# Optimization experiments

Measured on AMD Instinct MI355X. Metric: run time of the kernel, lower is better.

## Reference

```python
import jax, jax.numpy as jnp
import numpy as np

DIM = 768
NUM_HEADS = 12
HEAD_DIM = DIM // NUM_HEADS
B, N = 16, 784


def setup_inputs() -> dict:
    key = jax.random.key(0)
    k1, k2, k3, k4, k5 = jax.random.split(key, 5)
    x = jax.random.normal(k1, (B, N, DIM), dtype=jnp.float32)
    # Dense params (flax Dense: kernel [in, out], bias [out])
    Wqkv = jax.random.normal(k2, (DIM, 3 * DIM), dtype=jnp.float32) * (DIM ** -0.5)
    bqkv = jnp.zeros((3 * DIM,), dtype=jnp.float32)
    Wo = jax.random.normal(k3, (DIM, DIM), dtype=jnp.float32) * (DIM ** -0.5)
    bo = jnp.zeros((DIM,), dtype=jnp.float32)
    return {"x": x, "Wqkv": Wqkv, "bqkv": bqkv, "Wo": Wo, "bo": bo}


def reference(x, Wqkv, bqkv, Wo, bo):
    b, n, dim = x.shape
    # fused QKV projection
    qkv = jnp.einsum('bnd,df->bnf', x, Wqkv) + bqkv          # [b, n, 3*dim]
    qkv = qkv.reshape(b, n, 3, NUM_HEADS, HEAD_DIM)           # '(k h d)' split
    q, k, v = qkv[:, :, 0], qkv[:, :, 1], qkv[:, :, 2]        # [b, n, h, d]
    scale = HEAD_DIM ** -0.5
    # chunked/flash path computes exact softmax attention; same math, expressed densely
    scores = jnp.einsum('bihd,bjhd->bhij', q, k) * scale      # [b, h, n, n]
    attn = jax.nn.softmax(scores, axis=-1)
    out = jnp.einsum('bhij,bjhd->bihd', attn, v)              # [b, n, h, d]
    out = out.reshape(b, n, dim)                              # 'b n (h d)'
    return jnp.einsum('bnd,df->bnf', out, Wo) + bo
```

## Files before the change

kernel.cpp:

```cpp
#include <hip/hip_runtime.h>

#define DIM 768
#define NHEADS 12
#define HDIM 64
#define BB 16
#define NN 784
#define M_TOTAL (BB * NN)

typedef __attribute__((ext_vector_type(8))) _Float16 f16x8;
typedef __attribute__((ext_vector_type(4))) float f32x4;
typedef __attribute__((ext_vector_type(16))) float f32x16;

typedef __attribute__((address_space(3))) unsigned int lds_uint;
typedef __attribute__((address_space(1))) const unsigned int g_uint;
__device__ inline void gload_lds16(const void* g, void* l) {
    __builtin_amdgcn_global_load_lds((g_uint*)(uintptr_t)g,
                                     (lds_uint*)(uintptr_t)l, 16, 0, 0);
}

__global__ __launch_bounds__(256) void cvt_f16_kernel(
    const float* __restrict__ in, _Float16* __restrict__ out, int n)
{
    int i = (blockIdx.x * 256 + threadIdx.x) * 8;
    if (i >= n) return;
    float4 a = *(const float4*)&in[i];
    float4 b = *(const float4*)&in[i + 4];
    union { _Float16 h[8]; uint4 v; } o;
    o.h[0] = (_Float16)a.x; o.h[1] = (_Float16)a.y;
    o.h[2] = (_Float16)a.z; o.h[3] = (_Float16)a.w;
    o.h[4] = (_Float16)b.x; o.h[5] = (_Float16)b.y;
    o.h[6] = (_Float16)b.z; o.h[7] = (_Float16)b.w;
    *(uint4*)&out[i] = o.v;
}

__global__ __launch_bounds__(256) void transpose_f16_kernel(
    const float* __restrict__ W, _Float16* __restrict__ T, int K, int N)
{
    __shared__ float t[32][33];
    const int n0 = blockIdx.x * 32, k0 = blockIdx.y * 32;
    const int r = threadIdx.x >> 3, c4 = (threadIdx.x & 7) * 4;
    float4 v = *(const float4*)&W[(size_t)(k0 + r) * N + n0 + c4];
    t[r][c4 + 0] = v.x; t[r][c4 + 1] = v.y;
    t[r][c4 + 2] = v.z; t[r][c4 + 3] = v.w;
    __syncthreads();
    union { _Float16 h[4]; ushort4 v4; } o;
#pragma unroll
    for (int i = 0; i < 4; ++i) o.h[i] = (_Float16)t[c4 + i][r];
    *(ushort4*)&T[(size_t)(n0 + r) * K + k0 + c4] = o.v4;
}

template <int OUT_F16>
__global__ __launch_bounds__(256) void gemm_f16_kernel(
    const _Float16* __restrict__ A, const _Float16* __restrict__ B,
    const float* __restrict__ bias, void* __restrict__ Cout,
    int M, int N, int K)
{
    __shared__ _Float16 sA[128 * 64];
    __shared__ _Float16 sB[128 * 64];

    const int tid  = threadIdx.x;
    const int wave = tid >> 6;
    const int lane = tid & 63;
    const int gm = blockIdx.y * 128;
    const int gn = blockIdx.x * 128;
    const int wm = (wave & 1) * 64;
    const int wn = (wave >> 1) * 64;
    const int l31 = lane & 31;
    const int hi  = lane >> 5;

    const int srow = lane >> 3;
    const int scol = (((lane & 7) ^ (srow & 7)) * 8);

    f32x16 acc[2][2] = {};

    for (int k0 = 0; k0 < K; k0 += 64) {
        __syncthreads();
#pragma unroll
        for (int i = 0; i < 4; ++i) {
            const int rbase = wave * 32 + i * 8;
            gload_lds16(A + (size_t)(gm + rbase + srow) * K + k0 + scol,
                        &sA[rbase * 64]);
            gload_lds16(B + (size_t)(gn + rbase + srow) * K + k0 + scol,
                        &sB[rbase * 64]);
        }
        __syncthreads();

#pragma unroll
        for (int kk = 0; kk < 4; ++kk) {
            const int c = kk * 2 + hi;
            const int sw = (c ^ (l31 & 7)) * 8;
            f16x8 a[2], bf[2];
#pragma unroll
            for (int mt = 0; mt < 2; ++mt)
                a[mt] = *(const f16x8*)&sA[(wm + mt * 32 + l31) * 64 + sw];
#pragma unroll
            for (int nt = 0; nt < 2; ++nt)
                bf[nt] = *(const f16x8*)&sB[(wn + nt * 32 + l31) * 64 + sw];
#pragma unroll
            for (int mt = 0; mt < 2; ++mt)
#pragma unroll
                for (int nt = 0; nt < 2; ++nt)
                    acc[mt][nt] = __builtin_amdgcn_mfma_f32_32x32x16_f16(
                        a[mt], bf[nt], acc[mt][nt], 0, 0, 0);
        }
    }

#pragma unroll
    for (int nt = 0; nt < 2; ++nt) {
        const int col = gn + wn + nt * 32 + l31;
        const float bv = bias[col];
#pragma unroll
        for (int mt = 0; mt < 2; ++mt) {
            f32x16 v = acc[mt][nt];
#pragma unroll
            for (int reg = 0; reg < 16; ++reg) {
                const int row = gm + wm + mt * 32 + (reg & 3) + 8 * (reg >> 2) + 4 * hi;
                const float o = v[reg] + bv;
                if (OUT_F16)
                    ((_Float16*)Cout)[(size_t)row * N + col] = (_Float16)o;
                else
                    ((float*)Cout)[(size_t)row * N + col] = o;
            }
        }
    }
}

#define LOG2E_8 0.18033688f

#define ATTN_TILE(J0, TAIL)                                                    \
  {                                                                            \
    const int j0_ = (J0);                                                      \
    int jrowK = j0_ + sj;                                                      \
    if (TAIL && jrowK > NN - 1) jrowK = NN - 1;                                \
    const size_t kbase = (size_t)(b * NN + jrowK) * (3 * DIM) + DIM + h * HDIM;\
    uint4 k0v = *(const uint4*)&qkv[kbase + sg * 8];                           \
    uint4 k1v = *(const uint4*)&qkv[kbase + sg * 8 + 32];                      \
    int vr0 = j0_ + 2 * jj, vr1 = j0_ + 2 * jj + 1;                            \
    if (TAIL) { if (vr0 > NN - 1) vr0 = NN - 1; if (vr1 > NN - 1) vr1 = NN - 1; } \
    const size_t vb0 = (size_t)(b * NN + vr0) * (3 * DIM) + 2 * DIM + h * HDIM + dsub; \
    const size_t vb1 = (size_t)(b * NN + vr1) * (3 * DIM) + 2 * DIM + h * HDIM + dsub; \
    union { uint4 v; _Float16 h[8]; } va, vc;                                  \
    va.v = *(const uint4*)&qkv[vb0];                                           \
    vc.v = *(const uint4*)&qkv[vb1];                                           \
    __syncthreads();                                                           \
    *(uint4*)&Ks[sj][sg * 8]      = k0v;                                       \
    *(uint4*)&Ks[sj][sg * 8 + 32] = k1v;                                       \
    _Pragma("unroll")                                                          \
    for (int i = 0; i < 8; ++i) {                                              \
        union { _Float16 h[2]; unsigned int u; } t;                            \
        t.h[0] = va.h[i]; t.h[1] = vc.h[i];                                    \
        *(unsigned int*)&Vt[dsub + i][2 * jj] = t.u;                           \
    }                                                                          \
    __syncthreads();                                                           \
    f32x4 s[4] = {};                                                           \
    _Pragma("unroll")                                                          \
    for (int nt = 0; nt < 4; ++nt) {                                           \
        f16x8 kf0 = *(const f16x8*)&Ks[nt * 16 + l16][quad * 8];               \
        f16x8 kf1 = *(const f16x8*)&Ks[nt * 16 + l16][32 + quad * 8];          \
        s[nt] = __builtin_amdgcn_mfma_f32_16x16x32_f16(qfrag[0], kf0, s[nt], 0, 0, 0); \
        s[nt] = __builtin_amdgcn_mfma_f32_16x16x32_f16(qfrag[1], kf1, s[nt], 0, 0, 0); \
    }                                                                          \
    _Pragma("unroll")                                                          \
    for (int nt = 0; nt < 4; ++nt)                                             \
        _Pragma("unroll")                                                      \
        for (int r = 0; r < 4; ++r) {                                          \
            float pv = exp2f(s[nt][r]);                                        \
            if (TAIL && (j0_ + nt * 16) >= NN) pv = 0.f;                       \
            lpart[r] += pv;                                                    \
            Ph[wave * 16 + quad * 4 + r][nt * 16 + l16] = (_Float16)pv;        \
        }                                                                      \
    _Pragma("unroll")                                                          \
    for (int ks = 0; ks < 2; ++ks) {                                           \
        f16x8 ph = *(const f16x8*)&Ph[wave * 16 + l16][ks * 32 + quad * 8];    \
        _Pragma("unroll")                                                      \
        for (int dt = 0; dt < 4; ++dt) {                                       \
            f16x8 vf = *(const f16x8*)&Vt[dt * 16 + l16][ks * 32 + quad * 8];  \
            O[dt] = __builtin_amdgcn_mfma_f32_16x16x32_f16(ph, vf, O[dt], 0, 0, 0); \
        }                                                                      \
    }                                                                          \
  }

__global__ __launch_bounds__(256) void attn_f16_kernel(
    const _Float16* __restrict__ qkv, _Float16* __restrict__ oat)
{
    const int b = blockIdx.z;
    const int h = blockIdx.y;
    const int q0 = blockIdx.x * 64;
    const int tid = threadIdx.x;
    const int wave = tid >> 6;
    const int lane = tid & 63;
    const int quad = lane >> 4;
    const int l16  = lane & 15;

    __shared__ _Float16 Ks[64][72];
    __shared__ _Float16 Vt[64][72];
    __shared__ _Float16 Ph[64][72];

    f16x8 qfrag[2];
    {
        int qrow = q0 + wave * 16 + l16; if (qrow > NN - 1) qrow = NN - 1;
        size_t base = (size_t)(b * NN + qrow) * (3 * DIM) + h * HDIM;
        f16x8 q0v = *(const f16x8*)&qkv[base + quad * 8];
        f16x8 q1v = *(const f16x8*)&qkv[base + 32 + quad * 8];
        qfrag[0] = q0v * (_Float16)LOG2E_8;
        qfrag[1] = q1v * (_Float16)LOG2E_8;
    }

    const int sj = lane;
    const int sg = wave;
    const int jj   = lane & 31;
    const int dsub = sg * 16 + (lane >> 5) * 8;

    f32x4 O[4] = {};
    float lpart[4] = {};

    for (int jt = 0; jt < 12; ++jt) {
        ATTN_TILE(jt * 64, 0)
    }
    ATTN_TILE(768, 1)

    float lrow[4];
#pragma unroll
    for (int r = 0; r < 4; ++r) {
        float t = lpart[r];
        t += __shfl_xor(t, 1);
        t += __shfl_xor(t, 2);
        t += __shfl_xor(t, 4);
        t += __shfl_xor(t, 8);
        lrow[r] = t;
    }

#pragma unroll
    for (int r = 0; r < 4; ++r) {
        const int q = q0 + wave * 16 + quad * 4 + r;
        if (q < NN) {
            const float inv = 1.0f / lrow[r];
#pragma unroll
            for (int dt = 0; dt < 4; ++dt) {
                const size_t base = (size_t)(b * NN + q) * DIM + h * HDIM + dt * 16 + l16;
                oat[base] = (_Float16)(O[dt][r] * inv);
            }
        }
    }
}

extern "C" void kernel_launch(void* const* d_in, const int* in_sizes, int n_in,
                              void* d_out, int out_size, void* d_ws, size_t ws_size,
                              hipStream_t stream) {
    const float* x    = (const float*)d_in[0];
    const float* Wqkv = (const float*)d_in[1];
    const float* bqkv = (const float*)d_in[2];
    const float* Wo   = (const float*)d_in[3];
    const float* bo   = (const float*)d_in[4];
    float* out = (float*)d_out;

    _Float16* qkv = (_Float16*)d_ws;
    _Float16* xh  = qkv + (size_t)M_TOTAL * 3 * DIM;
    _Float16* wqT = xh + (size_t)M_TOTAL * DIM;
    _Float16* woT = wqT + (size_t)3 * DIM * DIM;
    _Float16* oat = xh;

    {
        int n = M_TOTAL * DIM;
        cvt_f16_kernel<<<n / 8 / 256, 256, 0, stream>>>(x, xh, n);
    }
    transpose_f16_kernel<<<dim3((3 * DIM) / 32, DIM / 32), 256, 0, stream>>>(
        Wqkv, wqT, DIM, 3 * DIM);
    transpose_f16_kernel<<<dim3(DIM / 32, DIM / 32), 256, 0, stream>>>(
        Wo, woT, DIM, DIM);
    gemm_f16_kernel<1><<<dim3((3 * DIM) / 128, M_TOTAL / 128), 256, 0, stream>>>(
        xh, wqT, bqkv, qkv, M_TOTAL, 3 * DIM, DIM);
    attn_f16_kernel<<<dim3(13, NHEADS, BB), 256, 0, stream>>>(qkv, oat);
    gemm_f16_kernel<0><<<dim3(DIM / 128, M_TOTAL / 128), 256, 0, stream>>>(
        oat, woT, bo, out, M_TOTAL, DIM, DIM);
}
```

Measured before the change: 276.9 us.

## Keep attention probabilities in registers and remap blocks across XCDs

```diff
diff --git a/kernel.cpp b/kernel.cpp
--- a/kernel.cpp
+++ b/kernel.cpp
@@ -149,7 +149,7 @@
     for (int i = 0; i < 8; ++i) {                                              \
         union { _Float16 h[2]; unsigned int u; } t;                            \
         t.h[0] = va.h[i]; t.h[1] = vc.h[i];                                    \
-        *(unsigned int*)&Vt[dsub + i][2 * jj] = t.u;                           \
+        *(unsigned int*)&Vt[dsub + i][pcol] = t.u;                             \
     }                                                                          \
     __syncthreads();                                                           \
     f32x4 s[4] = {};                                                           \
@@ -157,25 +157,34 @@
     for (int nt = 0; nt < 4; ++nt) {                                           \
         f16x8 kf0 = *(const f16x8*)&Ks[nt * 16 + l16][quad * 8];               \
         f16x8 kf1 = *(const f16x8*)&Ks[nt * 16 + l16][32 + quad * 8];          \
-        s[nt] = __builtin_amdgcn_mfma_f32_16x16x32_f16(qfrag[0], kf0, s[nt], 0, 0, 0); \
-        s[nt] = __builtin_amdgcn_mfma_f32_16x16x32_f16(qfrag[1], kf1, s[nt], 0, 0, 0); \
-    }                                                                          \
-    _Pragma("unroll")                                                          \
-    for (int nt = 0; nt < 4; ++nt)                                             \
+        s[nt] = __builtin_amdgcn_mfma_f32_16x16x32_f16(kf0, qfrag[0], s[nt], 0, 0, 0); \
+        s[nt] = __builtin_amdgcn_mfma_f32_16x16x32_f16(kf1, qfrag[1], s[nt], 0, 0, 0); \
+    }                                                                          \
+    unsigned int pk[4][2];                                                     \
+    _Pragma("unroll")                                                          \
+    for (int nt = 0; nt < 4; ++nt) {                                           \
+        float pv[4];                                                           \
         _Pragma("unroll")                                                      \
         for (int r = 0; r < 4; ++r) {                                          \
-            float pv = exp2f(s[nt][r]);                                        \
-            if (TAIL && (j0_ + nt * 16) >= NN) pv = 0.f;                       \
-            lpart[r] += pv;                                                    \
-            Ph[wave * 16 + quad * 4 + r][nt * 16 + l16] = (_Float16)pv;        \
+            float p = exp2f(s[nt][r]);                                         \
+            if (TAIL && (j0_ + nt * 16) >= NN) p = 0.f;                        \
+            lpart += p;                                                        \
+            pv[r] = p;                                                         \
         }                                                                      \
-    _Pragma("unroll")                                                          \
-    for (int ks = 0; ks < 2; ++ks) {                                           \
-        f16x8 ph = *(const f16x8*)&Ph[wave * 16 + l16][ks * 32 + quad * 8];    \
+        union { _Float16 h[2]; unsigned int u; } c0, c1;                       \
+        c0.h[0] = (_Float16)pv[0]; c0.h[1] = (_Float16)pv[1];                  \
+        c1.h[0] = (_Float16)pv[2]; c1.h[1] = (_Float16)pv[3];                  \
+        pk[nt][0] = c0.u; pk[nt][1] = c1.u;                                    \
+    }                                                                          \
+    _Pragma("unroll")                                                          \
+    for (int pc = 0; pc < 2; ++pc) {                                           \
+        union { unsigned int u[4]; f16x8 v; } pa;                              \
+        pa.u[0] = pk[2 * pc][0];     pa.u[1] = pk[2 * pc][1];                  \
+        pa.u[2] = pk[2 * pc + 1][0]; pa.u[3] = pk[2 * pc + 1][1];              \
         _Pragma("unroll")                                                      \
         for (int dt = 0; dt < 4; ++dt) {                                       \
-            f16x8 vf = *(const f16x8*)&Vt[dt * 16 + l16][ks * 32 + quad * 8];  \
-            O[dt] = __builtin_amdgcn_mfma_f32_16x16x32_f16(ph, vf, O[dt], 0, 0, 0); \
+            f16x8 vf = *(const f16x8*)&Vt[dt * 16 + l16][pc * 32 + quad * 8];  \
+            O[dt] = __builtin_amdgcn_mfma_f32_16x16x32_f16(pa.v, vf, O[dt], 0, 0, 0); \
         }                                                                      \
     }                                                                          \
   }
@@ -183,9 +192,13 @@
 __global__ __launch_bounds__(256) void attn_f16_kernel(
     const _Float16* __restrict__ qkv, _Float16* __restrict__ oat)
 {
-    const int b = blockIdx.z;
-    const int h = blockIdx.y;
-    const int q0 = blockIdx.x * 64;
+    const int L   = blockIdx.x + 13 * (blockIdx.y + NHEADS * blockIdx.z);
+    const int xcd = L & 7, ixc = L >> 3;
+    const int grp = xcd * 24 + ixc / 13;
+    const int q0  = (ixc % 13) * 64;
+    const int b   = grp / NHEADS;
+    const int h   = grp % NHEADS;
+
     const int tid = threadIdx.x;
     const int wave = tid >> 6;
     const int lane = tid & 63;
@@ -194,7 +207,6 @@
 
     __shared__ _Float16 Ks[64][72];
     __shared__ _Float16 Vt[64][72];
-    __shared__ _Float16 Ph[64][72];
 
     f16x8 qfrag[2];
     {
@@ -210,35 +222,33 @@
     const int sg = wave;
     const int jj   = lane & 31;
     const int dsub = sg * 16 + (lane >> 5) * 8;
+    const int pcol = ((jj >> 4) << 5) | (((jj >> 1) & 3) << 3)
+                   | (((jj >> 3) & 1) << 2) | ((jj & 1) << 1);
 
     f32x4 O[4] = {};
-    float lpart[4] = {};
+    float lpart = 0.f;
 
     for (int jt = 0; jt < 12; ++jt) {
         ATTN_TILE(jt * 64, 0)
     }
     ATTN_TILE(768, 1)
 
-    float lrow[4];
-#pragma unroll
-    for (int r = 0; r < 4; ++r) {
-        float t = lpart[r];
-        t += __shfl_xor(t, 1);
-        t += __shfl_xor(t, 2);
-        t += __shfl_xor(t, 4);
-        t += __shfl_xor(t, 8);
-        lrow[r] = t;
-    }
+    float t = lpart;
+    t += __shfl_xor(t, 16);
+    t += __shfl_xor(t, 32);
+    float inv[4];
+#pragma unroll
+    for (int r = 0; r < 4; ++r)
+        inv[r] = 1.0f / __shfl(t, quad * 4 + r, 16);
 
 #pragma unroll
     for (int r = 0; r < 4; ++r) {
         const int q = q0 + wave * 16 + quad * 4 + r;
         if (q < NN) {
-            const float inv = 1.0f / lrow[r];
 #pragma unroll
             for (int dt = 0; dt < 4; ++dt) {
                 const size_t base = (size_t)(b * NN + q) * DIM + h * HDIM + dt * 16 + l16;
-                oat[base] = (_Float16)(O[dt][r] * inv);
+                oat[base] = (_Float16)(O[dt][r] * inv[r]);
             }
         }
     }
```

New measurement: 265.3 us. 1.04x faster.
